# Kernel tuning notes

Measured on AMD Instinct MI355X. Metric: run time of the kernel, lower is better.

## Reference

```python
import jax, jax.numpy as jnp
import numpy as np

A = 1.0          # jacobi a
B = 1.0          # jacobi b
BASE_ALPHA = 2.0
K = 10           # polynomial order
N = 16384        # nodes
C = 32           # channels


def setup_inputs() -> dict:
    key = jax.random.key(0)
    k1, k2 = jax.random.split(key, 2)
    x = jax.random.normal(k1, (N, C), dtype=jnp.float32)
    # dense graph operator (stand-in for a normalized laplacian); scaled so spectrum is O(1)
    L = jax.random.normal(k2, (N, N), dtype=jnp.float32) / np.float32(np.sqrt(N))
    conv_params = jnp.full((K + 1,), min(1.0 / BASE_ALPHA, 1.0), dtype=jnp.float32)
    comb_params = jnp.ones((K + 1, C), dtype=jnp.float32)
    return {"x": x, "L": L, "conv_params": conv_params, "comb_params": comb_params}


def reference(x, L, conv_params, comb_params):
    a, b = A, B
    alpha = BASE_ALPHA * jnp.tanh(conv_params)  # [K+1] learned step sizes
    polys = [x]  # P_0 = x
    if K >= 1:
        # with l=-1, r=1: (r+l)/(r-l)=0, 1/(r-l)=0.5
        c1 = alpha[0] * (a - b) / 2.0
        c2 = alpha[0] * (a + b + 2.0) / 2.0
        polys.append(c1 * x + c2 * (L @ x))
    for i in range(2, K + 1):
        div = 2.0 * i * (i + a + b) * (2.0 * i + a + b - 2.0)
        r1 = (2.0 * i + a + b) * (2.0 * i + a + b - 1.0) * (2.0 * i + a + b - 2.0) / div
        r2 = (2.0 * i + a + b - 1.0) * (a * a - b * b) / div
        r3 = 2.0 * (i + a - 1.0) * (i + b - 1.0) * (2.0 * i + a + b) / div
        c1 = alpha[i - 1] * r1                      # multiplies L @ P_{i-1} (coef1, since 2/(r-l)=1)
        c2 = alpha[i - 1] * r2                      # coef2 (the (r+l)/(r-l) term vanishes)
        c3 = alpha[i - 1] * alpha[i - 2] * r3       # coef_3
        polys.append(c1 * (L @ polys[-1]) + c2 * polys[-1] - c3 * polys[-2])
    # y = sum_k comb[k] (broadcast over nodes) * P_k  -- avoids materializing the stacked [K+1,N,C]
    y = polys[0] * comb_params[0][None, :]
    for k in range(1, K + 1):
        y = y + comb_params[k][None, :] * polys[k]
    return y
```

## Files before the change

kernel.cpp:

```cpp
#include <hip/hip_runtime.h>
#include <math.h>


#define NN 16384
#define CC 32
#define KPOLY 10
#define NSPLIT 16
#define NTK (NN / 32)
#define WTILES 64

typedef _Float16 half8 __attribute__((ext_vector_type(8)));
typedef float f32x4 __attribute__((ext_vector_type(4)));
typedef unsigned int u32x4 __attribute__((ext_vector_type(4)));
typedef unsigned int u32x2 __attribute__((ext_vector_type(2)));

union U16 {
  u32x4 u;
  half8 h;
};
union H4 {
  _Float16 h[4];
  u32x2 u;
};

__global__ __launch_bounds__(256) void conv_pack_gemm1(const float* __restrict__ L,
                                                       _Float16* __restrict__ Lf,
                                                       const _Float16* __restrict__ Ph,
                                                       float* __restrict__ part) {
  __shared__ __align__(16) _Float16 lds[16 * 1024];
  const int tid = threadIdx.x;
  const int tr = blockIdx.x >> 4;
  const int sc = blockIdx.x & 15;
  const float* src = L + (size_t)tr * 16 * NN + (size_t)sc * 1024;

#pragma unroll
  for (int j = 0; j < 16; ++j) {
    const int flat = j * 256 + tid;
    const int r = flat >> 8;
    const int cu = flat & 255;
    f32x4 v = __builtin_nontemporal_load(
        reinterpret_cast<const f32x4*>(src + (size_t)r * NN) + cu);
    H4 o;
    o.h[0] = (_Float16)v.x;
    o.h[1] = (_Float16)v.y;
    o.h[2] = (_Float16)v.z;
    o.h[3] = (_Float16)v.w;
    const int u = (cu >> 1) ^ (r & 7);
    *reinterpret_cast<u32x2*>(&lds[r * 1024 + u * 8 + (cu & 1) * 4]) = o.u;
  }
  __syncthreads();

  const int lane = tid & 63;
  const int wave = tid >> 6;
  const int r = lane & 15;
  const int lg = lane >> 4;

  f32x4 acc0 = (f32x4){0.f, 0.f, 0.f, 0.f};
  f32x4 acc1 = (f32x4){0.f, 0.f, 0.f, 0.f};
#pragma unroll
  for (int i = 0; i < 8; ++i) {
    const int tkl = wave * 8 + i;
    const int u = (tkl * 4 + lg) ^ (r & 7);
    U16 aval;
    aval.u = *reinterpret_cast<const u32x4*>(&lds[r * 1024 + u * 8]);
    const size_t tk = (size_t)sc * 32 + tkl;
    __builtin_nontemporal_store(
        aval.u, reinterpret_cast<u32x4*>(Lf + ((size_t)tr * NTK + tk) * 512) + lane);
    const int kb = sc * 128 + tkl * 4 + lg;
    U16 b0, b1;
    b0.u = *reinterpret_cast<const u32x4*>(Ph + (size_t)kb * 256 + (size_t)r * 8);
    b1.u = *reinterpret_cast<const u32x4*>(Ph + (size_t)kb * 256 + (size_t)(16 + r) * 8);
    acc0 = __builtin_amdgcn_mfma_f32_16x16x32_f16(aval.h, b0.h, acc0, 0, 0, 0);
    acc1 = __builtin_amdgcn_mfma_f32_16x16x32_f16(aval.h, b1.h, acc1, 0, 0, 0);
  }
  __syncthreads();

  float* red = reinterpret_cast<float*>(lds);
#pragma unroll
  for (int j = 0; j < 4; ++j) {
    red[wave * 512 + (lg * 4 + j) * 32 + r] = acc0[j];
    red[wave * 512 + (lg * 4 + j) * 32 + 16 + r] = acc1[j];
  }
  __syncthreads();

  const int e = tid * 2;
  float2 s0 = *reinterpret_cast<const float2*>(&red[e]);
  float2 s1 = *reinterpret_cast<const float2*>(&red[512 + e]);
  float2 s2 = *reinterpret_cast<const float2*>(&red[1024 + e]);
  float2 s3 = *reinterpret_cast<const float2*>(&red[1536 + e]);
  float2 s = make_float2(s0.x + s1.x + s2.x + s3.x, s0.y + s1.y + s2.y + s3.y);
  *reinterpret_cast<float2*>(part + (size_t)sc * NN * CC + (size_t)tr * 16 * CC + e) = s;
}

__global__ __launch_bounds__(512, 1) void gemm_poly(
    const _Float16* __restrict__ Lf, const _Float16* __restrict__ PhIn,
    const float* __restrict__ Pprev, const float* __restrict__ Pprev2,
    float* __restrict__ Pnew, _Float16* __restrict__ PhOut, float* __restrict__ y,
    const float* __restrict__ conv, const float* __restrict__ comb_row, float r1,
    float r2, float r3, int ia, int ib) {
  const int tid = threadIdx.x;
  const int lane = tid & 63;
  const int wave = tid >> 6;
  const int trb = blockIdx.x * 4;
  const int l15 = lane & 15;
  const int lg = lane >> 4;
  const int tk0 = wave * WTILES;

  const u32x4* Ap[4];
#pragma unroll
  for (int rt = 0; rt < 4; ++rt)
    Ap[rt] = reinterpret_cast<const u32x4*>(
                 Lf + ((size_t)(trb + rt) * NTK + tk0) * 512) +
             lane;
  const _Float16* Bbase = PhIn + (size_t)(tk0 * 4 + lg) * 256 + (size_t)l15 * 8;

  f32x4 acc[4][2];
#pragma unroll
  for (int rt = 0; rt < 4; ++rt)
#pragma unroll
    for (int ct = 0; ct < 2; ++ct) acc[rt][ct] = (f32x4){0.f, 0.f, 0.f, 0.f};

  U16 A[2][4], B[2][2];
#pragma unroll
  for (int rt = 0; rt < 4; ++rt) A[0][rt].u = __builtin_nontemporal_load(Ap[rt]);
#pragma unroll
  for (int ct = 0; ct < 2; ++ct)
    B[0][ct].u = *reinterpret_cast<const u32x4*>(Bbase + ct * 128);

#pragma unroll
  for (int kk = 0; kk < WTILES; ++kk) {
    const int cur = kk & 1;
    const int nxt = cur ^ 1;
    if (kk < WTILES - 1) {
#pragma unroll
      for (int rt = 0; rt < 4; ++rt)
        A[nxt][rt].u = __builtin_nontemporal_load(Ap[rt] + (kk + 1) * 64);
#pragma unroll
      for (int ct = 0; ct < 2; ++ct)
        B[nxt][ct].u = *reinterpret_cast<const u32x4*>(
            Bbase + (size_t)(kk + 1) * 1024 + ct * 128);
    }
#pragma unroll
    for (int rt = 0; rt < 4; ++rt)
#pragma unroll
      for (int ct = 0; ct < 2; ++ct)
        acc[rt][ct] = __builtin_amdgcn_mfma_f32_16x16x32_f16(A[cur][rt].h, B[cur][ct].h,
                                                             acc[rt][ct], 0, 0, 0);
  }

  __shared__ float red[8][2048];
#pragma unroll
  for (int rt = 0; rt < 4; ++rt)
#pragma unroll
    for (int ct = 0; ct < 2; ++ct)
#pragma unroll
      for (int j = 0; j < 4; ++j)
        red[wave][(rt * 16 + lg * 4 + j) * 32 + ct * 16 + l15] = acc[rt][ct][j];
  __syncthreads();

  const int e0 = tid * 4;
  float4 t = make_float4(0.f, 0.f, 0.f, 0.f);
#pragma unroll
  for (int w = 0; w < 8; ++w) {
    float4 p = *reinterpret_cast<const float4*>(&red[w][e0]);
    t.x += p.x;
    t.y += p.y;
    t.z += p.z;
    t.w += p.w;
  }

  const int row = e0 >> 5;
  const int c = e0 & 31;
  const int n = blockIdx.x * 64 + row;
  const size_t g = (size_t)n * CC + c;

  const float a1 = 2.f * tanhf(conv[ia]);
  const float a2 = 2.f * tanhf(conv[ib]);
  const float cL = a1 * r1;
  const float cP = a1 * r2;
  const float cPP = a1 * a2 * r3;

  float4 pp = *reinterpret_cast<const float4*>(Pprev + g);
  float4 p2 = *reinterpret_cast<const float4*>(Pprev2 + g);
  float4 pn;
  pn.x = cL * t.x + cP * pp.x - cPP * p2.x;
  pn.y = cL * t.y + cP * pp.y - cPP * p2.y;
  pn.z = cL * t.z + cP * pp.z - cPP * p2.z;
  pn.w = cL * t.w + cP * pp.w - cPP * p2.w;
  *reinterpret_cast<float4*>(Pnew + g) = pn;

  const size_t pb = (size_t)(n >> 3) * 256 + (size_t)c * 8 + (n & 7);
  PhOut[pb] = (_Float16)pn.x;
  PhOut[pb + 8] = (_Float16)pn.y;
  PhOut[pb + 16] = (_Float16)pn.z;
  PhOut[pb + 24] = (_Float16)pn.w;

  float4 cb = *reinterpret_cast<const float4*>(comb_row + c);
  float4 yv = *reinterpret_cast<float4*>(y + g);
  yv.x = fmaf(cb.x, pn.x, yv.x);
  yv.y = fmaf(cb.y, pn.y, yv.y);
  yv.z = fmaf(cb.z, pn.z, yv.z);
  yv.w = fmaf(cb.w, pn.w, yv.w);
  *reinterpret_cast<float4*>(y + g) = yv;
}

__global__ __launch_bounds__(256) void init_kernel(const float* __restrict__ x,
                                                   const float* __restrict__ comb,
                                                   float* __restrict__ y,
                                                   _Float16* __restrict__ Ph) {
  int idx = blockIdx.x * blockDim.x + threadIdx.x;
  float4 xv = reinterpret_cast<const float4*>(x)[idx];
  int c4 = (idx & 7) << 2;
  int n = idx >> 3;
  float4 cb = *reinterpret_cast<const float4*>(comb + c4);
  reinterpret_cast<float4*>(y)[idx] =
      make_float4(xv.x * cb.x, xv.y * cb.y, xv.z * cb.z, xv.w * cb.w);
  size_t pb = (size_t)(n >> 3) * 256 + (size_t)c4 * 8 + (n & 7);
  Ph[pb] = (_Float16)xv.x;
  Ph[pb + 8] = (_Float16)xv.y;
  Ph[pb + 16] = (_Float16)xv.z;
  Ph[pb + 24] = (_Float16)xv.w;
}

__global__ __launch_bounds__(256) void poly_update(
    const float* __restrict__ part, float* __restrict__ Pnew,
    const float* __restrict__ Pprev, float* __restrict__ y,
    _Float16* __restrict__ PhOut, const float* __restrict__ conv,
    const float* __restrict__ comb_row, float r1, float r2, int ia) {
  int idx = blockIdx.x * blockDim.x + threadIdx.x;
  float a1 = 2.f * tanhf(conv[ia]);
  float cL = a1 * r1;
  float cP = a1 * r2;

  float4 t = make_float4(0.f, 0.f, 0.f, 0.f);
#pragma unroll
  for (int s = 0; s < NSPLIT; ++s) {
    float4 p = reinterpret_cast<const float4*>(part)[(size_t)s * (NN * CC / 4) + idx];
    t.x += p.x;
    t.y += p.y;
    t.z += p.z;
    t.w += p.w;
  }

  float4 pp = reinterpret_cast<const float4*>(Pprev)[idx];
  float4 pn;
  pn.x = cL * t.x + cP * pp.x;
  pn.y = cL * t.y + cP * pp.y;
  pn.z = cL * t.z + cP * pp.z;
  pn.w = cL * t.w + cP * pp.w;
  reinterpret_cast<float4*>(Pnew)[idx] = pn;

  int c4 = (idx & 7) << 2;
  int n = idx >> 3;
  size_t pb = (size_t)(n >> 3) * 256 + (size_t)c4 * 8 + (n & 7);
  PhOut[pb] = (_Float16)pn.x;
  PhOut[pb + 8] = (_Float16)pn.y;
  PhOut[pb + 16] = (_Float16)pn.z;
  PhOut[pb + 24] = (_Float16)pn.w;

  float4 cb = *reinterpret_cast<const float4*>(comb_row + c4);
  float4 yv = reinterpret_cast<float4*>(y)[idx];
  yv.x = fmaf(cb.x, pn.x, yv.x);
  yv.y = fmaf(cb.y, pn.y, yv.y);
  yv.z = fmaf(cb.z, pn.z, yv.z);
  yv.w = fmaf(cb.w, pn.w, yv.w);
  reinterpret_cast<float4*>(y)[idx] = yv;
}

static void jacobi_r(int i, double a, double b, float& r1, float& r2, float& r3) {
  double div = 2.0 * i * (i + a + b) * (2.0 * i + a + b - 2.0);
  r1 = (float)((2.0 * i + a + b) * (2.0 * i + a + b - 1.0) * (2.0 * i + a + b - 2.0) / div);
  r2 = (float)((2.0 * i + a + b - 1.0) * (a * a - b * b) / div);
  r3 = (float)(2.0 * (i + a - 1.0) * (i + b - 1.0) * (2.0 * i + a + b) / div);
}

extern "C" void kernel_launch(void* const* d_in, const int* in_sizes, int n_in,
                              void* d_out, int out_size, void* d_ws, size_t ws_size,
                              hipStream_t stream) {
  const float* x = (const float*)d_in[0];
  const float* Lm = (const float*)d_in[1];
  const float* conv = (const float*)d_in[2];
  const float* comb = (const float*)d_in[3];
  float* y = (float*)d_out;
  char* ws = (char*)d_ws;

  _Float16* Lf = (_Float16*)ws;
  float* part = (float*)(ws + 536870912ull);
  _Float16* PhA = (_Float16*)(ws + 536870912ull + 33554432ull);
  _Float16* PhB = PhA + (size_t)NN * CC;
  float* Pb0 = (float*)(ws + 536870912ull + 33554432ull + 4194304ull);
  float* Pb1 = Pb0 + (size_t)NN * CC;
  float* Pb2 = Pb1 + (size_t)NN * CC;
  float* bufs[3] = {Pb0, Pb1, Pb2};

  const double Aj = 1.0, Bj = 1.0;
  const int ew_blocks = NN * CC / 4 / 256;

  init_kernel<<<ew_blocks, 256, 0, stream>>>(x, comb, y, PhA);
  conv_pack_gemm1<<<16384, 256, 0, stream>>>(Lm, Lf, PhA, part);

  {
    float r1 = (float)((Aj + Bj + 2.0) / 2.0);
    float r2 = (float)((Aj - Bj) / 2.0);
    poly_update<<<ew_blocks, 256, 0, stream>>>(part, bufs[0], x, y, PhB, conv,
                                               comb + CC, r1, r2, 0);
  }

  const float* Pprev = bufs[0];
  const float* Pprev2 = x;
  for (int i = 2; i <= KPOLY; ++i) {
    float r1, r2, r3;
    jacobi_r(i, Aj, Bj, r1, r2, r3);
    float* Pn = bufs[(i - 1) % 3];
    const _Float16* PhIn = (i & 1) ? PhA : PhB;
    _Float16* PhOut = (i & 1) ? PhB : PhA;
    gemm_poly<<<NN / 64, 512, 0, stream>>>(Lf, PhIn, Pprev, Pprev2, Pn, PhOut, y,
                                           conv, comb + (size_t)i * CC, r1, r2, r3,
                                           i - 1, i - 2);
    Pprev2 = Pprev;
    Pprev = Pn;
  }
}
```

Before: 1.127 ms.

## Fuse Jacobi recurrence GEMMs into one persistent kernel with grid barriers

Replaces the nine per-order gemm_poly launches with a single persistent kernel of 256 blocks. The blocks synchronise between polynomial orders with an atomic-counter grid barrier. The previous two polynomials and the y accumulator stay in registers across iterations, so the fp32 P buffers and the per-step y read-modify-write go away and y is written once at the end. This targets launch gaps and redundant elementwise memory traffic. It relies on all 256 blocks being co-resident and adds the cost of a spin-wait barrier after each order.

```diff
diff --git a/kernel.cpp b/kernel.cpp
--- a/kernel.cpp
+++ b/kernel.cpp
@@ -8,6 +8,7 @@
 #define NSPLIT 16
 #define NTK (NN / 32)
 #define WTILES 64
+#define NBLK 256
 
 typedef _Float16 half8 __attribute__((ext_vector_type(8)));
 typedef float f32x4 __attribute__((ext_vector_type(4)));
@@ -21,6 +22,12 @@
 union H4 {
   _Float16 h[4];
   u32x2 u;
+};
+
+struct Coefs {
+  float r1[KPOLY + 1];
+  float r2[KPOLY + 1];
+  float r3[KPOLY + 1];
 };
 
 __global__ __launch_bounds__(256) void conv_pack_gemm1(const float* __restrict__ L,
@@ -92,12 +99,25 @@
   *reinterpret_cast<float2*>(part + (size_t)sc * NN * CC + (size_t)tr * 16 * CC + e) = s;
 }
 
-__global__ __launch_bounds__(512, 1) void gemm_poly(
-    const _Float16* __restrict__ Lf, const _Float16* __restrict__ PhIn,
-    const float* __restrict__ Pprev, const float* __restrict__ Pprev2,
-    float* __restrict__ Pnew, _Float16* __restrict__ PhOut, float* __restrict__ y,
-    const float* __restrict__ conv, const float* __restrict__ comb_row, float r1,
-    float r2, float r3, int ia, int ib) {
+__device__ __forceinline__ void gridbar(unsigned* cnt, unsigned target) {
+  __syncthreads();
+  if (threadIdx.x == 0) {
+    __threadfence();
+    __hip_atomic_fetch_add(cnt, 1u, __ATOMIC_ACQ_REL, __HIP_MEMORY_SCOPE_AGENT);
+    while (__hip_atomic_load(cnt, __ATOMIC_ACQUIRE, __HIP_MEMORY_SCOPE_AGENT) < target) {
+      __builtin_amdgcn_s_sleep(8);
+    }
+    __threadfence();
+  }
+  __syncthreads();
+}
+
+__global__ __launch_bounds__(512, 1) void gemm_poly_persist(
+    const _Float16* __restrict__ Lf, _Float16* __restrict__ PhA,
+    _Float16* __restrict__ PhB, const float* __restrict__ x,
+    const float* __restrict__ P1, float* __restrict__ y,
+    const float* __restrict__ conv, const float* __restrict__ comb,
+    unsigned* __restrict__ cnt, Coefs cf) {
   const int tid = threadIdx.x;
   const int lane = tid & 63;
   const int wave = tid >> 6;
@@ -112,114 +132,127 @@
     Ap[rt] = reinterpret_cast<const u32x4*>(
                  Lf + ((size_t)(trb + rt) * NTK + tk0) * 512) +
              lane;
-  const _Float16* Bbase = PhIn + (size_t)(tk0 * 4 + lg) * 256 + (size_t)l15 * 8;
-
-  f32x4 acc[4][2];
-#pragma unroll
-  for (int rt = 0; rt < 4; ++rt)
-#pragma unroll
-    for (int ct = 0; ct < 2; ++ct) acc[rt][ct] = (f32x4){0.f, 0.f, 0.f, 0.f};
-
-  U16 A[2][4], B[2][2];
-#pragma unroll
-  for (int rt = 0; rt < 4; ++rt) A[0][rt].u = __builtin_nontemporal_load(Ap[rt]);
-#pragma unroll
-  for (int ct = 0; ct < 2; ++ct)
-    B[0][ct].u = *reinterpret_cast<const u32x4*>(Bbase + ct * 128);
-
-#pragma unroll
-  for (int kk = 0; kk < WTILES; ++kk) {
-    const int cur = kk & 1;
-    const int nxt = cur ^ 1;
-    if (kk < WTILES - 1) {
-#pragma unroll
-      for (int rt = 0; rt < 4; ++rt)
-        A[nxt][rt].u = __builtin_nontemporal_load(Ap[rt] + (kk + 1) * 64);
-#pragma unroll
-      for (int ct = 0; ct < 2; ++ct)
-        B[nxt][ct].u = *reinterpret_cast<const u32x4*>(
-            Bbase + (size_t)(kk + 1) * 1024 + ct * 128);
-    }
-#pragma unroll
-    for (int rt = 0; rt < 4; ++rt)
-#pragma unroll
-      for (int ct = 0; ct < 2; ++ct)
-        acc[rt][ct] = __builtin_amdgcn_mfma_f32_16x16x32_f16(A[cur][rt].h, B[cur][ct].h,
-                                                             acc[rt][ct], 0, 0, 0);
-  }
-
-  __shared__ float red[8][2048];
-#pragma unroll
-  for (int rt = 0; rt < 4; ++rt)
-#pragma unroll
-    for (int ct = 0; ct < 2; ++ct)
-#pragma unroll
-      for (int j = 0; j < 4; ++j)
-        red[wave][(rt * 16 + lg * 4 + j) * 32 + ct * 16 + l15] = acc[rt][ct][j];
-  __syncthreads();
 
   const int e0 = tid * 4;
-  float4 t = make_float4(0.f, 0.f, 0.f, 0.f);
-#pragma unroll
-  for (int w = 0; w < 8; ++w) {
-    float4 p = *reinterpret_cast<const float4*>(&red[w][e0]);
-    t.x += p.x;
-    t.y += p.y;
-    t.z += p.z;
-    t.w += p.w;
-  }
-
   const int row = e0 >> 5;
   const int c = e0 & 31;
   const int n = blockIdx.x * 64 + row;
   const size_t g = (size_t)n * CC + c;
-
-  const float a1 = 2.f * tanhf(conv[ia]);
-  const float a2 = 2.f * tanhf(conv[ib]);
-  const float cL = a1 * r1;
-  const float cP = a1 * r2;
-  const float cPP = a1 * a2 * r3;
-
-  float4 pp = *reinterpret_cast<const float4*>(Pprev + g);
-  float4 p2 = *reinterpret_cast<const float4*>(Pprev2 + g);
-  float4 pn;
-  pn.x = cL * t.x + cP * pp.x - cPP * p2.x;
-  pn.y = cL * t.y + cP * pp.y - cPP * p2.y;
-  pn.z = cL * t.z + cP * pp.z - cPP * p2.z;
-  pn.w = cL * t.w + cP * pp.w - cPP * p2.w;
-  *reinterpret_cast<float4*>(Pnew + g) = pn;
-
   const size_t pb = (size_t)(n >> 3) * 256 + (size_t)c * 8 + (n & 7);
-  PhOut[pb] = (_Float16)pn.x;
-  PhOut[pb + 8] = (_Float16)pn.y;
-  PhOut[pb + 16] = (_Float16)pn.z;
-  PhOut[pb + 24] = (_Float16)pn.w;
-
-  float4 cb = *reinterpret_cast<const float4*>(comb_row + c);
-  float4 yv = *reinterpret_cast<float4*>(y + g);
-  yv.x = fmaf(cb.x, pn.x, yv.x);
-  yv.y = fmaf(cb.y, pn.y, yv.y);
-  yv.z = fmaf(cb.z, pn.z, yv.z);
-  yv.w = fmaf(cb.w, pn.w, yv.w);
-  *reinterpret_cast<float4*>(y + g) = yv;
+  float4 pp = *reinterpret_cast<const float4*>(P1 + g);
+  float4 p2 = *reinterpret_cast<const float4*>(x + g);
+  float4 yacc = *reinterpret_cast<const float4*>(y + g);
+
+  __shared__ float red[8][2048];
+
+  for (int i = 2; i <= KPOLY; ++i) {
+    const _Float16* PhIn = (i & 1) ? PhA : PhB;
+    _Float16* PhOut = (i & 1) ? PhB : PhA;
+    const _Float16* Bbase = PhIn + (size_t)(tk0 * 4 + lg) * 256 + (size_t)l15 * 8;
+
+    f32x4 acc[4][2];
+#pragma unroll
+    for (int rt = 0; rt < 4; ++rt)
+#pragma unroll
+      for (int ct = 0; ct < 2; ++ct) acc[rt][ct] = (f32x4){0.f, 0.f, 0.f, 0.f};
+
+    U16 A[2][4], B[2][2];
+#pragma unroll
+    for (int rt = 0; rt < 4; ++rt) A[0][rt].u = __builtin_nontemporal_load(Ap[rt]);
+#pragma unroll
+    for (int ct = 0; ct < 2; ++ct)
+      B[0][ct].u = *reinterpret_cast<const u32x4*>(Bbase + ct * 128);
+
+#pragma unroll
+    for (int kk = 0; kk < WTILES; ++kk) {
+      const int cur = kk & 1;
+      const int nxt = cur ^ 1;
+      if (kk < WTILES - 1) {
+#pragma unroll
+        for (int rt = 0; rt < 4; ++rt)
+          A[nxt][rt].u = __builtin_nontemporal_load(Ap[rt] + (kk + 1) * 64);
+#pragma unroll
+        for (int ct = 0; ct < 2; ++ct)
+          B[nxt][ct].u = *reinterpret_cast<const u32x4*>(
+              Bbase + (size_t)(kk + 1) * 1024 + ct * 128);
+      }
+#pragma unroll
+      for (int rt = 0; rt < 4; ++rt)
+#pragma unroll
+        for (int ct = 0; ct < 2; ++ct)
+          acc[rt][ct] = __builtin_amdgcn_mfma_f32_16x16x32_f16(
+              A[cur][rt].h, B[cur][ct].h, acc[rt][ct], 0, 0, 0);
+    }
+
+#pragma unroll
+    for (int rt = 0; rt < 4; ++rt)
+#pragma unroll
+      for (int ct = 0; ct < 2; ++ct)
+#pragma unroll
+        for (int j = 0; j < 4; ++j)
+          red[wave][(rt * 16 + lg * 4 + j) * 32 + ct * 16 + l15] = acc[rt][ct][j];
+    __syncthreads();
+
+    float4 t = make_float4(0.f, 0.f, 0.f, 0.f);
+#pragma unroll
+    for (int w = 0; w < 8; ++w) {
+      float4 p = *reinterpret_cast<const float4*>(&red[w][e0]);
+      t.x += p.x;
+      t.y += p.y;
+      t.z += p.z;
+      t.w += p.w;
+    }
+
+    const float a1 = 2.f * tanhf(conv[i - 1]);
+    const float a2 = 2.f * tanhf(conv[i - 2]);
+    const float cL = a1 * cf.r1[i];
+    const float cP = a1 * cf.r2[i];
+    const float cPP = a1 * a2 * cf.r3[i];
+
+    float4 pn;
+    pn.x = cL * t.x + cP * pp.x - cPP * p2.x;
+    pn.y = cL * t.y + cP * pp.y - cPP * p2.y;
+    pn.z = cL * t.z + cP * pp.z - cPP * p2.z;
+    pn.w = cL * t.w + cP * pp.w - cPP * p2.w;
+
+    PhOut[pb] = (_Float16)pn.x;
+    PhOut[pb + 8] = (_Float16)pn.y;
+    PhOut[pb + 16] = (_Float16)pn.z;
+    PhOut[pb + 24] = (_Float16)pn.w;
+
+    const float4 cb = *reinterpret_cast<const float4*>(comb + (size_t)i * CC + c);
+    yacc.x = fmaf(cb.x, pn.x, yacc.x);
+    yacc.y = fmaf(cb.y, pn.y, yacc.y);
+    yacc.z = fmaf(cb.z, pn.z, yacc.z);
+    yacc.w = fmaf(cb.w, pn.w, yacc.w);
+
+    p2 = pp;
+    pp = pn;
+
+    if (i < KPOLY) gridbar(cnt, (unsigned)(i - 1) * NBLK);
+  }
+
+  *reinterpret_cast<float4*>(y + g) = yacc;
 }
 
 __global__ __launch_bounds__(256) void init_kernel(const float* __restrict__ x,
                                                    const float* __restrict__ comb,
                                                    float* __restrict__ y,
-                                                   _Float16* __restrict__ Ph) {
+                                                   _Float16* __restrict__ Ph,
+                                                   unsigned* __restrict__ cnt) {
   int idx = blockIdx.x * blockDim.x + threadIdx.x;
+  if (idx == 0) __hip_atomic_store(cnt, 0u, __ATOMIC_RELAXED, __HIP_MEMORY_SCOPE_AGENT);
   float4 xv = reinterpret_cast<const float4*>(x)[idx];
   int c4 = (idx & 7) << 2;
   int n = idx >> 3;
   float4 cb = *reinterpret_cast<const float4*>(comb + c4);
   reinterpret_cast<float4*>(y)[idx] =
       make_float4(xv.x * cb.x, xv.y * cb.y, xv.z * cb.z, xv.w * cb.w);
-  size_t pb = (size_t)(n >> 3) * 256 + (size_t)c4 * 8 + (n & 7);
-  Ph[pb] = (_Float16)xv.x;
-  Ph[pb + 8] = (_Float16)xv.y;
-  Ph[pb + 16] = (_Float16)xv.z;
-  Ph[pb + 24] = (_Float16)xv.w;
+  size_t pbi = (size_t)(n >> 3) * 256 + (size_t)c4 * 8 + (n & 7);
+  Ph[pbi] = (_Float16)xv.x;
+  Ph[pbi + 8] = (_Float16)xv.y;
+  Ph[pbi + 16] = (_Float16)xv.z;
+  Ph[pbi + 24] = (_Float16)xv.w;
 }
 
 __global__ __launch_bounds__(256) void poly_update(
@@ -252,11 +285,11 @@
 
   int c4 = (idx & 7) << 2;
   int n = idx >> 3;
-  size_t pb = (size_t)(n >> 3) * 256 + (size_t)c4 * 8 + (n & 7);
-  PhOut[pb] = (_Float16)pn.x;
-  PhOut[pb + 8] = (_Float16)pn.y;
-  PhOut[pb + 16] = (_Float16)pn.z;
-  PhOut[pb + 24] = (_Float16)pn.w;
+  size_t pbi = (size_t)(n >> 3) * 256 + (size_t)c4 * 8 + (n & 7);
+  PhOut[pbi] = (_Float16)pn.x;
+  PhOut[pbi + 8] = (_Float16)pn.y;
+  PhOut[pbi + 16] = (_Float16)pn.z;
+  PhOut[pbi + 24] = (_Float16)pn.w;
 
   float4 cb = *reinterpret_cast<const float4*>(comb_row + c4);
   float4 yv = reinterpret_cast<float4*>(y)[idx];
@@ -289,35 +322,27 @@
   _Float16* PhA = (_Float16*)(ws + 536870912ull + 33554432ull);
   _Float16* PhB = PhA + (size_t)NN * CC;
   float* Pb0 = (float*)(ws + 536870912ull + 33554432ull + 4194304ull);
-  float* Pb1 = Pb0 + (size_t)NN * CC;
-  float* Pb2 = Pb1 + (size_t)NN * CC;
-  float* bufs[3] = {Pb0, Pb1, Pb2};
+  unsigned* cnt = (unsigned*)(ws + 536870912ull + 33554432ull + 4194304ull + 2097152ull);
 
   const double Aj = 1.0, Bj = 1.0;
   const int ew_blocks = NN * CC / 4 / 256;
 
-  init_kernel<<<ew_blocks, 256, 0, stream>>>(x, comb, y, PhA);
+  Coefs cf;
+  for (int i = 0; i <= KPOLY; ++i) {
+    cf.r1[i] = cf.r2[i] = cf.r3[i] = 0.f;
+    if (i >= 2) jacobi_r(i, Aj, Bj, cf.r1[i], cf.r2[i], cf.r3[i]);
+  }
+
+  init_kernel<<<ew_blocks, 256, 0, stream>>>(x, comb, y, PhA, cnt);
   conv_pack_gemm1<<<16384, 256, 0, stream>>>(Lm, Lf, PhA, part);
 
   {
     float r1 = (float)((Aj + Bj + 2.0) / 2.0);
     float r2 = (float)((Aj - Bj) / 2.0);
-    poly_update<<<ew_blocks, 256, 0, stream>>>(part, bufs[0], x, y, PhB, conv,
+    poly_update<<<ew_blocks, 256, 0, stream>>>(part, Pb0, x, y, PhB, conv,
                                                comb + CC, r1, r2, 0);
   }
 
-  const float* Pprev = bufs[0];
-  const float* Pprev2 = x;
-  for (int i = 2; i <= KPOLY; ++i) {
-    float r1, r2, r3;
-    jacobi_r(i, Aj, Bj, r1, r2, r3);
-    float* Pn = bufs[(i - 1) % 3];
-    const _Float16* PhIn = (i & 1) ? PhA : PhB;
-    _Float16* PhOut = (i & 1) ? PhB : PhA;
-    gemm_poly<<<NN / 64, 512, 0, stream>>>(Lf, PhIn, Pprev, Pprev2, Pn, PhOut, y,
-                                           conv, comb + (size_t)i * CC, r1, r2, r3,
-                                           i - 1, i - 2);
-    Pprev2 = Pprev;
-    Pprev = Pn;
-  }
-}
+  gemm_poly_persist<<<NBLK, 512, 0, stream>>>(Lf, PhA, PhB, x, Pb0, y, conv, comb,
+                                              cnt, cf);
+}
```

New measurement: 1.968 ms. 1.75x slower.
